# Kernel tuning notes

Measured on AMD Instinct MI355X. Metric: run time of the kernel, lower is better.

Reference implementation:

```python
import jax, jax.numpy as jnp
import numpy as np

DIM_HEAD = 32  # from init_kwargs; scale = dim_head**-0.5 per the Triton kernel


def setup_inputs() -> dict:
    key = jax.random.key(0)
    k1, k2 = jax.random.split(key)
    B, N, dim = 16, 8192, 128
    D = 4 * DIM_HEAD  # heads * dim_head
    x = jax.random.normal(k1, (B, N, dim), dtype=jnp.float32)
    # ParameterList of 16 stages, each Parameter is randn(2, dim, D) * 0.02
    qk_weights = jax.random.normal(k2, (16, 2, dim, D), dtype=jnp.float32) * 0.02
    return {"x": x, "qk_weights": qk_weights}


def reference(x, qk_weights):
    """FFT-inspired butterfly attention.

    At stage s (stride = 2**s), positions are grouped into blocks of 2*stride;
    the first `stride` elements of each block are 'a', the next `stride` are
    their butterfly partners 'b' (b = a + stride). Q/K are projected from the
    ORIGINAL x with per-stage weights; v is the running value buffer (init x).
    For each pair, a 2-way softmax over [qa.ka, qa.kb] mixes (va, vb).
    """
    B, N, dim = x.shape
    logN = int(round(np.log2(N)))
    D = qk_weights.shape[-1]
    scale = DIM_HEAD ** -0.5

    v = x
    for s in range(logN):
        stride = 1 << s
        Wq = qk_weights[s, 0]  # (dim, D)
        Wk = qk_weights[s, 1]
        q = jnp.einsum('bnd,de->bne', x, Wq) * scale  # (B,N,D)
        k = jnp.einsum('bnd,de->bne', x, Wk)
        G = N // (2 * stride)
        qr = q.reshape(B, G, 2, stride, D)
        kr = k.reshape(B, G, 2, stride, D)
        vr = v.reshape(B, G, 2, stride, dim)
        qa = qr[:, :, 0]
        ka, kb = kr[:, :, 0], kr[:, :, 1]
        va, vb = vr[:, :, 0], vr[:, :, 1]
        s_aa = jnp.sum(qa * ka, axis=-1)  # (B,G,stride)
        s_ab = jnp.sum(qa * kb, axis=-1)
        attn = jax.nn.softmax(jnp.stack([s_aa, s_ab], axis=-1), axis=-1)
        w0 = attn[..., 0:1]
        w1 = attn[..., 1:2]
        out_a = w0 * va + w1 * vb
        out_b = w1 * va + w0 * vb
        v = jnp.stack([out_a, out_b], axis=2).reshape(B, N, dim)
    return v
```

## Files before the change

### kernel.cpp

```cpp
#include <hip/hip_runtime.h>
#include <hip/hip_bf16.h>


typedef __bf16 bf16x8 __attribute__((ext_vector_type(8)));
typedef float  f32x4  __attribute__((ext_vector_type(4)));

#define XSTR 136
#define XB_BYTES  (128 * XSTR * 2)
#define PREP_LDS  (2 * XB_BYTES)

#define XW 128
#define XB_SWZ    (128 * XW * 2)
#define WT_LDS_OFF XB_SWZ
#define LDS_FUSED (XB_SWZ + 7 * 4 * 64 * 4)

__device__ __forceinline__ float ubits(unsigned int u) {
    union { unsigned int u; float f; } v; v.u = u; return v.f;
}
__device__ __forceinline__ unsigned short f2bf(float f) {
    union { float f; unsigned int u; } v; v.f = f;
    unsigned int u = v.u;
    return (unsigned short)((u + 0x7fffu + ((u >> 16) & 1u)) >> 16);
}
__device__ __forceinline__ unsigned int cvtpk(float lo, float hi) {
    unsigned int r;
    asm("v_cvt_pk_bf16_f32 %0, %1, %2" : "=v"(r) : "v"(lo), "v"(hi));
    return r;
}
__device__ __forceinline__ int swzr(int r) { return ((r >> 1) ^ (r >> 2)) & 15; }

#define DPP_MOV_F(x, ctrl) \
    __int_as_float(__builtin_amdgcn_update_dpp(0, __float_as_int(x), (ctrl), 0xF, 0xF, true))

__device__ __forceinline__ float xlane_u(float x, int u, int lane) {
    if (u == 0) return DPP_MOV_F(x, 0xB1);
    if (u == 1) return DPP_MOV_F(x, 0x4E);
    if (u == 2) return __int_as_float(__builtin_amdgcn_ds_swizzle(__float_as_int(x), 0x101F));
    if (u == 3) return __int_as_float(__builtin_amdgcn_ds_swizzle(__float_as_int(x), 0x201F));
    if (u == 4) return __int_as_float(__builtin_amdgcn_ds_swizzle(__float_as_int(x), 0x401F));
    return __int_as_float(__builtin_amdgcn_ds_bpermute((lane ^ 32) << 2, __float_as_int(x)));
}

__global__ __launch_bounds__(512)
void prep_kernel(const float* __restrict__ qkw, unsigned short* __restrict__ PT) {
    extern __shared__ char smem[];
    unsigned short* wkb = (unsigned short*)smem;
    unsigned short* wqb = (unsigned short*)(smem + XB_BYTES);
    const int s = blockIdx.x;
    const float* Wq = qkw + (size_t)s * 32768;
    const float* Wk = Wq + 16384;
    const int tid = threadIdx.x;
    const int rl = tid >> 5, c4 = tid & 31;
#pragma unroll
    for (int j = 0; j < 8; ++j) {
        int r = j * 16 + rl;
        float4 vq = ((const float4*)Wq)[r * 32 + c4];
        float4 vk = ((const float4*)Wk)[r * 32 + c4];
        uint2 uq; uq.x = cvtpk(vq.x, vq.y); uq.y = cvtpk(vq.z, vq.w);
        uint2 uk; uk.x = cvtpk(vk.x, vk.y); uk.y = cvtpk(vk.z, vk.w);
        *(uint2*)(wqb + r * XSTR + c4 * 4) = uq;
        *(uint2*)(wkb + r * XSTR + c4 * 4) = uk;
    }
    __syncthreads();
    const int lane = tid & 63, w = tid >> 6;
    const int lane15 = lane & 15, quad = lane >> 4;
    f32x4 acc[8] = {};
#pragma unroll
    for (int kk = 0; kk < 4; ++kk) {
        bf16x8 a = *(const bf16x8*)(wkb + (w * 16 + lane15) * XSTR + kk * 32 + quad * 8);
#pragma unroll
        for (int ct = 0; ct < 8; ++ct) {
            bf16x8 b = *(const bf16x8*)(wqb + (ct * 16 + lane15) * XSTR + kk * 32 + quad * 8);
            acc[ct] = __builtin_amdgcn_mfma_f32_16x16x32_bf16(a, b, acc[ct], 0, 0, 0);
        }
    }
    unsigned short* dst = PT + s * 16384;
#pragma unroll
    for (int ct = 0; ct < 8; ++ct) {
        const int kkf = ct >> 1;
        const int qf  = (ct & 1) * 2 + (lane15 >> 3);
        const int e   = lane15 & 7;
#pragma unroll
        for (int r = 0; r < 4; ++r) {
            int fi = (w * 4 + kkf) * 64 + qf * 16 + quad * 4 + r;
            dst[fi * 8 + e] = f2bf(acc[ct][r] * 0.17677669529663687f);
        }
    }
}

__device__ __forceinline__ void stage_xb_swz(unsigned short* xb, const float* xsrc,
                                             int tid, int base, int h_off, int rstride) {
    const int rl = tid >> 5, c4 = tid & 31;
#pragma unroll
    for (int j = 0; j < 8; ++j) {
        int i  = j * 16 + rl;
        int gp = base + (i >> 6) * h_off + (i & 63) * rstride;
        float4 val = ((const float4*)xsrc)[gp * 32 + c4];
        uint2 us; us.x = cvtpk(val.x, val.y); us.y = cvtpk(val.z, val.w);
        int slot = c4 >> 1, half = c4 & 1;
        *(uint2*)(xb + i * XW + (((slot ^ swzr(i)) << 3) + half * 4)) = us;
    }
}

template<int NS>
__global__ __launch_bounds__(512, 4)
void fused_kernel(const float* __restrict__ xsrc,
                  const float* __restrict__ vsrc,
                  float* __restrict__ vdst,
                  const unsigned short* __restrict__ PT,
                  int s0, int base_mul, int h_off, int rstride)
{
    extern __shared__ char smem[];
    unsigned short* xb  = (unsigned short*)smem;
    float*          wtl = (float*)(smem + WT_LDS_OFF);

    const int tid  = threadIdx.x;
    const int b    = blockIdx.x >> 6;
    const int sub  = blockIdx.x & 63;
    const int base = b * 8192 + sub * base_mul;

    stage_xb_swz(xb, xsrc, tid, base, h_off, rstride);

    const int lane = tid & 63, w = tid >> 6;
    const int lane15 = lane & 15, quad = lane >> 4;
    const int dh = w >> 1;
    const int ph = w & 1;

    uint4 af[2][2][4];
    {
        const uint4* Pf = (const uint4*)PT + (size_t)s0 * 2048;
#pragma unroll
        for (int mt = 0; mt < 2; ++mt)
#pragma unroll
            for (int kk = 0; kk < 4; ++kk)
                af[0][mt][kk] = Pf[((dh * 2 + mt) * 4 + kk) * 64 + lane];
    }
    __syncthreads();

#pragma unroll
    for (int u = 0; u < NS; ++u) {
        const int cur = u & 1, nxt = cur ^ 1;
        const int t   = 1 << u;
        const int tm1 = t - 1;

        if (u + 1 < NS) {
            const uint4* Pf = (const uint4*)PT + (size_t)(s0 + u + 1) * 2048;
#pragma unroll
            for (int mt = 0; mt < 2; ++mt)
#pragma unroll
                for (int kk = 0; kk < 4; ++kk)
                    af[nxt][mt][kk] = Pf[((dh * 2 + mt) * 4 + kk) * 64 + lane];
        }

        f32x4 acc[2][2] = {};
#pragma unroll
        for (int pg = 0; pg < 2; ++pg) {
            const int p  = (ph * 2 + pg) * 16 + lane15;
            const int ar = ((p & ~tm1) << 1) | (p & tm1);
            const int swa = swzr(ar);
            const unsigned short* brow = xb + ar * XW;
#pragma unroll
            for (int kk = 0; kk < 4; ++kk) {
                bf16x8 bfrag = *(const bf16x8*)(brow + (((kk * 4 + quad) ^ swa) << 3));
#pragma unroll
                for (int mt = 0; mt < 2; ++mt) {
                    union { uint4 u; bf16x8 b; } av; av.u = af[cur][mt][kk];
                    acc[mt][pg] = __builtin_amdgcn_mfma_f32_16x16x32_bf16(av.b, bfrag, acc[mt][pg], 0, 0, 0);
                }
            }
        }

        float sm[2];
#pragma unroll
        for (int pg = 0; pg < 2; ++pg) {
            const int p  = (ph * 2 + pg) * 16 + lane15;
            const int ar = ((p & ~tm1) << 1) | (p & tm1);
            const int br = ar + t;
            const int swa = swzr(ar), swb = swzr(br);
            float s = 0.f;
#pragma unroll
            for (int mt = 0; mt < 2; ++mt) {
                const int slot = dh * 4 + mt * 2 + (quad >> 1);
                uint2 ua = *(const uint2*)(xb + ar * XW + (((slot ^ swa) << 3) + (quad & 1) * 4));
                uint2 ub = *(const uint2*)(xb + br * XW + (((slot ^ swb) << 3) + (quad & 1) * 4));
                float a0 = ubits(ua.x << 16), a1 = ubits(ua.x & 0xffff0000u);
                float a2 = ubits(ua.y << 16), a3 = ubits(ua.y & 0xffff0000u);
                float b0 = ubits(ub.x << 16), b1 = ubits(ub.x & 0xffff0000u);
                float b2 = ubits(ub.y << 16), b3 = ubits(ub.y & 0xffff0000u);
                s += acc[mt][pg][0] * (a0 - b0) + acc[mt][pg][1] * (a1 - b1)
                   + acc[mt][pg][2] * (a2 - b2) + acc[mt][pg][3] * (a3 - b3);
            }
            s += xlane_u(s, 4, lane);
            s += xlane_u(s, 5, lane);
            sm[pg] = s;
        }
        float v = (lane & 16) ? sm[1] : sm[0];
        if (lane < 32)
            wtl[(u * 4 + dh) * 64 + ph * 32 + (lane & 31)] = v;
    }
    __syncthreads();

    float dlt[NS];
#pragma unroll
    for (int u = 0; u < NS; ++u) {
        dlt[u] = wtl[(u * 4 + 0) * 64 + lane] + wtl[(u * 4 + 1) * 64 + lane]
               + wtl[(u * 4 + 2) * 64 + lane] + wtl[(u * 4 + 3) * 64 + lane];
    }

    float vlo[16], vhi[16];
    {
        int r0 = 2 * lane, r1 = r0 + 1;
        int gp0 = base + (r0 >> 6) * h_off + (r0 & 63) * rstride;
        int gp1 = base + (r1 >> 6) * h_off + (r1 & 63) * rstride;
        const float* p0 = vsrc + (size_t)gp0 * 128 + w * 16;
        const float* p1 = vsrc + (size_t)gp1 * 128 + w * 16;
#pragma unroll
        for (int j = 0; j < 4; ++j) {
            float4 a = ((const float4*)p0)[j];
            float4 c = ((const float4*)p1)[j];
            vlo[4*j] = a.x; vlo[4*j+1] = a.y; vlo[4*j+2] = a.z; vlo[4*j+3] = a.w;
            vhi[4*j] = c.x; vhi[4*j+1] = c.y; vhi[4*j+2] = c.z; vhi[4*j+3] = c.w;
        }
    }

#pragma unroll
    for (int u = 0; u < NS; ++u) {
        const float w0 = 1.0f / (1.0f + __expf(-dlt[u]));
        if (u < NS - 1) {
            const bool isE = ((lane >> u) & 1) == 0;
            const float wk = isE ? w0 : 1.0f - w0;
#pragma unroll
            for (int j = 0; j < 16; ++j) {
                float a = vlo[j], c = vhi[j];
                float s    = a + c;
                float keep = c + wk * (a - c);
                float send = s - keep;
                float ex   = xlane_u(send, u, lane);
                vlo[j] = isE ? keep : ex;
                vhi[j] = isE ? ex : keep;
            }
        } else {
            const float w1 = 1.0f - w0;
#pragma unroll
            for (int j = 0; j < 16; ++j) {
                float a = vlo[j], c = vhi[j];
                float oa = w0 * a + w1 * c;
                vlo[j] = oa;
                vhi[j] = a + c - oa;
            }
        }
    }

    float* vbuf = (float*)smem;
    const int FU = NS - 1;
    const int r0 = ((lane >> FU) << (FU + 1)) | (lane & ((1 << FU) - 1));
    const int r1 = r0 + (1 << FU);
    const int rl = tid >> 5, c4 = tid & 31;
#pragma unroll
    for (int pass = 0; pass < 2; ++pass) {
        if (pass) __syncthreads();
        if ((r0 >> 6) == pass) {
            const int lr = r0 & 63;
#pragma unroll
            for (int j = 0; j < 4; ++j) {
                float4 a; a.x = vlo[4*j]; a.y = vlo[4*j+1]; a.z = vlo[4*j+2]; a.w = vlo[4*j+3];
                *(float4*)(vbuf + lr * 128 + (((w * 4 + j) ^ (lr & 31)) << 2)) = a;
            }
        }
        if ((r1 >> 6) == pass) {
            const int lr = r1 & 63;
#pragma unroll
            for (int j = 0; j < 4; ++j) {
                float4 c; c.x = vhi[4*j]; c.y = vhi[4*j+1]; c.z = vhi[4*j+2]; c.w = vhi[4*j+3];
                *(float4*)(vbuf + lr * 128 + (((w * 4 + j) ^ (lr & 31)) << 2)) = c;
            }
        }
        __syncthreads();
#pragma unroll
        for (int j = 0; j < 4; ++j) {
            int i  = j * 16 + rl;
            int gr = pass * 64 + i;
            int gp = base + (gr >> 6) * h_off + (gr & 63) * rstride;
            ((float4*)vdst)[gp * 32 + c4] =
                *(const float4*)(vbuf + i * 128 + ((c4 ^ (i & 31)) << 2));
        }
    }
}

extern "C" void kernel_launch(void* const* d_in, const int* in_sizes, int n_in,
                              void* d_out, int out_size, void* d_ws, size_t ws_size,
                              hipStream_t stream) {
    const float* x   = (const float*)d_in[0];
    const float* qkw = (const float*)d_in[1];
    float* out = (float*)d_out;
    unsigned short* PT = (unsigned short*)d_ws;

    (void)hipFuncSetAttribute((const void*)prep_kernel,
                              hipFuncAttributeMaxDynamicSharedMemorySize, PREP_LDS);
    (void)hipFuncSetAttribute((const void*)fused_kernel<7>,
                              hipFuncAttributeMaxDynamicSharedMemorySize, LDS_FUSED);
    (void)hipFuncSetAttribute((const void*)fused_kernel<6>,
                              hipFuncAttributeMaxDynamicSharedMemorySize, LDS_FUSED);

    prep_kernel<<<13, 512, PREP_LDS, stream>>>(qkw, PT);

    fused_kernel<7><<<1024, 512, LDS_FUSED, stream>>>(
        x, x, out, PT, 0, 128, 64, 1);

    fused_kernel<6><<<1024, 512, LDS_FUSED, stream>>>(
        x, out, out, PT, 7, 2, 1, 128);
}
```

Before: 197.2 us.

## Double fused kernel block size to 1024 threads, halving per-warp work

Launches the fused butterfly kernels with 16 waves per block instead of 8. Each wave now handles one 16-pair group for the score MFMAs and 8 columns of the value mixing, so per-thread register use and serial work drop. Warp-to-data mapping for scores, partial sums and output staging is rewritten to match. The cost is more threads per block contending for LDS and barriers, plus possible occupancy limits from the larger launch bound.

Result: slower. 222.0 us (+12.6%).

```diff
diff --git a/kernel.cpp b/kernel.cpp
--- a/kernel.cpp
+++ b/kernel.cpp
@@ -88,22 +88,8 @@
     }
 }
 
-__device__ __forceinline__ void stage_xb_swz(unsigned short* xb, const float* xsrc,
-                                             int tid, int base, int h_off, int rstride) {
-    const int rl = tid >> 5, c4 = tid & 31;
-#pragma unroll
-    for (int j = 0; j < 8; ++j) {
-        int i  = j * 16 + rl;
-        int gp = base + (i >> 6) * h_off + (i & 63) * rstride;
-        float4 val = ((const float4*)xsrc)[gp * 32 + c4];
-        uint2 us; us.x = cvtpk(val.x, val.y); us.y = cvtpk(val.z, val.w);
-        int slot = c4 >> 1, half = c4 & 1;
-        *(uint2*)(xb + i * XW + (((slot ^ swzr(i)) << 3) + half * 4)) = us;
-    }
-}
-
 template<int NS>
-__global__ __launch_bounds__(512, 4)
+__global__ __launch_bounds__(1024, 8)
 void fused_kernel(const float* __restrict__ xsrc,
                   const float* __restrict__ vsrc,
                   float* __restrict__ vdst,
@@ -119,12 +105,23 @@
     const int sub  = blockIdx.x & 63;
     const int base = b * 8192 + sub * base_mul;
 
-    stage_xb_swz(xb, xsrc, tid, base, h_off, rstride);
+    {
+        const int rl = tid >> 5, c4 = tid & 31;
+#pragma unroll
+        for (int j = 0; j < 4; ++j) {
+            int i  = j * 32 + rl;
+            int gp = base + (i >> 6) * h_off + (i & 63) * rstride;
+            float4 val = ((const float4*)xsrc)[gp * 32 + c4];
+            uint2 us; us.x = cvtpk(val.x, val.y); us.y = cvtpk(val.z, val.w);
+            int slot = c4 >> 1, half = c4 & 1;
+            *(uint2*)(xb + i * XW + (((slot ^ swzr(i)) << 3) + half * 4)) = us;
+        }
+    }
 
     const int lane = tid & 63, w = tid >> 6;
     const int lane15 = lane & 15, quad = lane >> 4;
-    const int dh = w >> 1;
-    const int ph = w & 1;
+    const int dg = w >> 2;
+    const int ph = w & 3;
 
     uint4 af[2][2][4];
     {
@@ -133,7 +130,7 @@
         for (int mt = 0; mt < 2; ++mt)
 #pragma unroll
             for (int kk = 0; kk < 4; ++kk)
-                af[0][mt][kk] = Pf[((dh * 2 + mt) * 4 + kk) * 64 + lane];
+                af[0][mt][kk] = Pf[((dg * 2 + mt) * 4 + kk) * 64 + lane];
     }
     __syncthreads();
 
@@ -149,54 +146,43 @@
             for (int mt = 0; mt < 2; ++mt)
 #pragma unroll
                 for (int kk = 0; kk < 4; ++kk)
-                    af[nxt][mt][kk] = Pf[((dh * 2 + mt) * 4 + kk) * 64 + lane];
-        }
-
-        f32x4 acc[2][2] = {};
-#pragma unroll
-        for (int pg = 0; pg < 2; ++pg) {
-            const int p  = (ph * 2 + pg) * 16 + lane15;
-            const int ar = ((p & ~tm1) << 1) | (p & tm1);
-            const int swa = swzr(ar);
-            const unsigned short* brow = xb + ar * XW;
-#pragma unroll
-            for (int kk = 0; kk < 4; ++kk) {
-                bf16x8 bfrag = *(const bf16x8*)(brow + (((kk * 4 + quad) ^ swa) << 3));
-#pragma unroll
-                for (int mt = 0; mt < 2; ++mt) {
-                    union { uint4 u; bf16x8 b; } av; av.u = af[cur][mt][kk];
-                    acc[mt][pg] = __builtin_amdgcn_mfma_f32_16x16x32_bf16(av.b, bfrag, acc[mt][pg], 0, 0, 0);
-                }
-            }
-        }
-
-        float sm[2];
-#pragma unroll
-        for (int pg = 0; pg < 2; ++pg) {
-            const int p  = (ph * 2 + pg) * 16 + lane15;
-            const int ar = ((p & ~tm1) << 1) | (p & tm1);
-            const int br = ar + t;
-            const int swa = swzr(ar), swb = swzr(br);
-            float s = 0.f;
+                    af[nxt][mt][kk] = Pf[((dg * 2 + mt) * 4 + kk) * 64 + lane];
+        }
+
+        const int p  = ph * 16 + lane15;
+        const int ar = ((p & ~tm1) << 1) | (p & tm1);
+        const int swa = swzr(ar);
+        const unsigned short* brow = xb + ar * XW;
+        f32x4 acc[2] = {};
+#pragma unroll
+        for (int kk = 0; kk < 4; ++kk) {
+            bf16x8 bfrag = *(const bf16x8*)(brow + (((kk * 4 + quad) ^ swa) << 3));
 #pragma unroll
             for (int mt = 0; mt < 2; ++mt) {
-                const int slot = dh * 4 + mt * 2 + (quad >> 1);
-                uint2 ua = *(const uint2*)(xb + ar * XW + (((slot ^ swa) << 3) + (quad & 1) * 4));
-                uint2 ub = *(const uint2*)(xb + br * XW + (((slot ^ swb) << 3) + (quad & 1) * 4));
-                float a0 = ubits(ua.x << 16), a1 = ubits(ua.x & 0xffff0000u);
-                float a2 = ubits(ua.y << 16), a3 = ubits(ua.y & 0xffff0000u);
-                float b0 = ubits(ub.x << 16), b1 = ubits(ub.x & 0xffff0000u);
-                float b2 = ubits(ub.y << 16), b3 = ubits(ub.y & 0xffff0000u);
-                s += acc[mt][pg][0] * (a0 - b0) + acc[mt][pg][1] * (a1 - b1)
-                   + acc[mt][pg][2] * (a2 - b2) + acc[mt][pg][3] * (a3 - b3);
-            }
-            s += xlane_u(s, 4, lane);
-            s += xlane_u(s, 5, lane);
-            sm[pg] = s;
-        }
-        float v = (lane & 16) ? sm[1] : sm[0];
-        if (lane < 32)
-            wtl[(u * 4 + dh) * 64 + ph * 32 + (lane & 31)] = v;
+                union { uint4 u; bf16x8 b; } av; av.u = af[cur][mt][kk];
+                acc[mt] = __builtin_amdgcn_mfma_f32_16x16x32_bf16(av.b, bfrag, acc[mt], 0, 0, 0);
+            }
+        }
+
+        const int br  = ar + t;
+        const int swb = swzr(br);
+        float s = 0.f;
+#pragma unroll
+        for (int mt = 0; mt < 2; ++mt) {
+            const int slot = (dg * 2 + mt) * 2 + (quad >> 1);
+            uint2 ua = *(const uint2*)(xb + ar * XW + (((slot ^ swa) << 3) + (quad & 1) * 4));
+            uint2 ub = *(const uint2*)(xb + br * XW + (((slot ^ swb) << 3) + (quad & 1) * 4));
+            float a0 = ubits(ua.x << 16), a1 = ubits(ua.x & 0xffff0000u);
+            float a2 = ubits(ua.y << 16), a3 = ubits(ua.y & 0xffff0000u);
+            float b0 = ubits(ub.x << 16), b1 = ubits(ub.x & 0xffff0000u);
+            float b2 = ubits(ub.y << 16), b3 = ubits(ub.y & 0xffff0000u);
+            s += acc[mt][0] * (a0 - b0) + acc[mt][1] * (a1 - b1)
+               + acc[mt][2] * (a2 - b2) + acc[mt][3] * (a3 - b3);
+        }
+        s += xlane_u(s, 4, lane);
+        s += xlane_u(s, 5, lane);
+        if (lane < 16)
+            wtl[(u * 4 + dg) * 64 + ph * 16 + lane] = s;
     }
     __syncthreads();
 
@@ -207,15 +193,15 @@
                + wtl[(u * 4 + 2) * 64 + lane] + wtl[(u * 4 + 3) * 64 + lane];
     }
 
-    float vlo[16], vhi[16];
+    float vlo[8], vhi[8];
     {
         int r0 = 2 * lane, r1 = r0 + 1;
         int gp0 = base + (r0 >> 6) * h_off + (r0 & 63) * rstride;
         int gp1 = base + (r1 >> 6) * h_off + (r1 & 63) * rstride;
-        const float* p0 = vsrc + (size_t)gp0 * 128 + w * 16;
-        const float* p1 = vsrc + (size_t)gp1 * 128 + w * 16;
-#pragma unroll
-        for (int j = 0; j < 4; ++j) {
+        const float* p0 = vsrc + (size_t)gp0 * 128 + w * 8;
+        const float* p1 = vsrc + (size_t)gp1 * 128 + w * 8;
+#pragma unroll
+        for (int j = 0; j < 2; ++j) {
             float4 a = ((const float4*)p0)[j];
             float4 c = ((const float4*)p1)[j];
             vlo[4*j] = a.x; vlo[4*j+1] = a.y; vlo[4*j+2] = a.z; vlo[4*j+3] = a.w;
@@ -230,7 +216,7 @@
             const bool isE = ((lane >> u) & 1) == 0;
             const float wk = isE ? w0 : 1.0f - w0;
 #pragma unroll
-            for (int j = 0; j < 16; ++j) {
+            for (int j = 0; j < 8; ++j) {
                 float a = vlo[j], c = vhi[j];
                 float s    = a + c;
                 float keep = c + wk * (a - c);
@@ -242,7 +228,7 @@
         } else {
             const float w1 = 1.0f - w0;
 #pragma unroll
-            for (int j = 0; j < 16; ++j) {
+            for (int j = 0; j < 8; ++j) {
                 float a = vlo[j], c = vhi[j];
                 float oa = w0 * a + w1 * c;
                 vlo[j] = oa;
@@ -262,23 +248,23 @@
         if ((r0 >> 6) == pass) {
             const int lr = r0 & 63;
 #pragma unroll
-            for (int j = 0; j < 4; ++j) {
+            for (int j = 0; j < 2; ++j) {
                 float4 a; a.x = vlo[4*j]; a.y = vlo[4*j+1]; a.z = vlo[4*j+2]; a.w = vlo[4*j+3];
-                *(float4*)(vbuf + lr * 128 + (((w * 4 + j) ^ (lr & 31)) << 2)) = a;
+                *(float4*)(vbuf + lr * 128 + (((w * 2 + j) ^ (lr & 31)) << 2)) = a;
             }
         }
         if ((r1 >> 6) == pass) {
             const int lr = r1 & 63;
 #pragma unroll
-            for (int j = 0; j < 4; ++j) {
+            for (int j = 0; j < 2; ++j) {
                 float4 c; c.x = vhi[4*j]; c.y = vhi[4*j+1]; c.z = vhi[4*j+2]; c.w = vhi[4*j+3];
-                *(float4*)(vbuf + lr * 128 + (((w * 4 + j) ^ (lr & 31)) << 2)) = c;
+                *(float4*)(vbuf + lr * 128 + (((w * 2 + j) ^ (lr & 31)) << 2)) = c;
             }
         }
         __syncthreads();
 #pragma unroll
-        for (int j = 0; j < 4; ++j) {
-            int i  = j * 16 + rl;
+        for (int j = 0; j < 2; ++j) {
+            int i  = j * 32 + rl;
             int gr = pass * 64 + i;
             int gp = base + (gr >> 6) * h_off + (gr & 63) * rstride;
             ((float4*)vdst)[gp * 32 + c4] =
@@ -304,9 +290,9 @@
 
     prep_kernel<<<13, 512, PREP_LDS, stream>>>(qkw, PT);
 
-    fused_kernel<7><<<1024, 512, LDS_FUSED, stream>>>(
+    fused_kernel<7><<<1024, 1024, LDS_FUSED, stream>>>(
         x, x, out, PT, 0, 128, 64, 1);
 
-    fused_kernel<6><<<1024, 512, LDS_FUSED, stream>>>(
+    fused_kernel<6><<<1024, 1024, LDS_FUSED, stream>>>(
         x, out, out, PT, 7, 2, 1, 128);
 }
```
